# Kernel optimization log

Measured on AMD Instinct MI355X. Metric: run time of the kernel, lower is better.

## Reference

```python
import jax, jax.numpy as jnp
import numpy as np

X_DIM, Y_DIM, HIDDEN, N = 768, 768, 300, 768


def setup_inputs() -> dict:
    key = jax.random.key(0)
    ks = jax.random.split(key, 7)
    lim1 = 1.0 / np.sqrt(X_DIM + Y_DIM)
    lim2 = 1.0 / np.sqrt(HIDDEN)
    return {
        "x_samples": jax.random.normal(ks[0], (N, X_DIM), dtype=jnp.float32),
        "y_samples": jax.random.normal(ks[1], (N, Y_DIM), dtype=jnp.float32),
        "perm": jax.random.permutation(ks[2], N).astype(jnp.int32),
        # Linear 1: (x_dim+y_dim) -> hidden, torch default uniform init
        "W1": jax.random.uniform(ks[3], (HIDDEN, X_DIM + Y_DIM), jnp.float32, -lim1, lim1),
        "b1": jax.random.uniform(ks[4], (HIDDEN,), jnp.float32, -lim1, lim1),
        # Linear 2: hidden -> 1
        "W2": jax.random.uniform(ks[5], (1, HIDDEN), jnp.float32, -lim2, lim2),
        "b2": jax.random.uniform(ks[6], (1,), jnp.float32, -lim2, lim2),
    }


def reference(x_samples, y_samples, perm, W1, b1, W2, b2):
    n = x_samples.shape[0]
    x_dim = x_samples.shape[1]
    # First linear is separable across the concat: split W1 into x- and y-parts.
    hx = x_samples @ W1[:, :x_dim].T            # [N, H]
    hy = y_samples @ W1[:, x_dim:].T            # [N, H]
    w2 = W2[0]                                   # [H]
    # T0: matched pairs (x_i, y_i)
    t0 = jax.nn.softplus(jax.nn.relu(hx + hy + b1) @ w2 + b2[0])   # [N]
    # T1[i, j] = F(x_j, y_perm[i]) -- pairwise tile, [N, N, H] intermediate
    hyp = hy[perm]                               # [N, H]
    hpair = jax.nn.relu(hyp[:, None, :] + hx[None, :, :] + b1)     # [N, N, H]
    t1 = jax.nn.softplus(hpair @ w2 + b2[0])     # [N, N]
    lower_bound = t0.mean() - (jax.nn.logsumexp(t1, axis=1).mean() - jnp.log(n).astype(t1.dtype))
    return lower_bound
```

## Files before the change

### kernel.cpp

```cpp
#include <hip/hip_runtime.h>
#include <math.h>

#define NN   768
#define HH   300
#define HPAD 320
#define KD   768

#define P_OFF    0
#define PKS_STR  245760
#define PG_STR   1966080
#define CF_OFF   3932160
#define AF_OFF   4177920
#define SP_OFF   4423680
#define SP_STR   589824
#define ES_OFF   6782976
#define T0_OFF   6783744

__global__ __launch_bounds__(256) void k1_gemm(
    const float* __restrict__ x, const float* __restrict__ y,
    const int* __restrict__ perm, const float* __restrict__ W1,
    float* __restrict__ wsf)
{
    const int tid = threadIdx.x;
    const int tx = tid & 15;
    const int ty = tid >> 4;
    const int i0 = blockIdx.x * 128;
    const int h0 = blockIdx.y * 64;
    const int g  = blockIdx.z & 1;
    const int ks = blockIdx.z >> 1;
    const int kbeg = ks * 96;

    const float* src = g ? y : x;
    const int koff = g ? KD : 0;

    __shared__ float Xt[32][132];
    __shared__ float Wt[32][68];

    float4 acc[4][2];
    #pragma unroll
    for (int r = 0; r < 4; ++r) { acc[r][0] = make_float4(0,0,0,0);
                                  acc[r][1] = make_float4(0,0,0,0); }

    const int kq = (tid & 7) << 2;
    const float* xp[4];
    int xr[4];
    #pragma unroll
    for (int it = 0; it < 4; ++it) {
        int row = ((tid + it*256) >> 3);
        int gr = i0 + row;
        if (g) gr = perm[gr];
        xp[it] = src + (size_t)gr * KD + kbeg + kq;
        xr[it] = row;
    }
    const float* wp[2];
    int wr[2]; bool wv[2];
    #pragma unroll
    for (int it = 0; it < 2; ++it) {
        int hrow = ((tid + it*256) >> 3);
        int hg = h0 + hrow;
        wv[it] = hg < HH;
        wp[it] = W1 + (size_t)(wv[it] ? hg : 0) * (2*KD) + koff + kbeg + kq;
        wr[it] = hrow;
    }

    for (int kb = 0; kb < 96; kb += 32) {
        float4 xv[4], wvv[2];
        #pragma unroll
        for (int it = 0; it < 4; ++it) xv[it] = *(const float4*)(xp[it] + kb);
        #pragma unroll
        for (int it = 0; it < 2; ++it) {
            wvv[it] = *(const float4*)(wp[it] + kb);
            if (!wv[it]) wvv[it] = make_float4(0,0,0,0);
        }
        if (kb) __syncthreads();
        #pragma unroll
        for (int it = 0; it < 4; ++it) {
            Xt[kq+0][xr[it]] = xv[it].x; Xt[kq+1][xr[it]] = xv[it].y;
            Xt[kq+2][xr[it]] = xv[it].z; Xt[kq+3][xr[it]] = xv[it].w;
        }
        #pragma unroll
        for (int it = 0; it < 2; ++it) {
            Wt[kq+0][wr[it]] = wvv[it].x; Wt[kq+1][wr[it]] = wvv[it].y;
            Wt[kq+2][wr[it]] = wvv[it].z; Wt[kq+3][wr[it]] = wvv[it].w;
        }
        __syncthreads();

        #pragma unroll 8
        for (int k = 0; k < 32; ++k) {
            float4 a  = *(const float4*)&Wt[k][4*ty];
            float4 b0 = *(const float4*)&Xt[k][4*tx];
            float4 b1v = *(const float4*)&Xt[k][64 + 4*tx];
            float ar[4] = {a.x, a.y, a.z, a.w};
            #pragma unroll
            for (int r = 0; r < 4; ++r) {
                acc[r][0].x = fmaf(ar[r], b0.x,  acc[r][0].x);
                acc[r][0].y = fmaf(ar[r], b0.y,  acc[r][0].y);
                acc[r][0].z = fmaf(ar[r], b0.z,  acc[r][0].z);
                acc[r][0].w = fmaf(ar[r], b0.w,  acc[r][0].w);
                acc[r][1].x = fmaf(ar[r], b1v.x, acc[r][1].x);
                acc[r][1].y = fmaf(ar[r], b1v.y, acc[r][1].y);
                acc[r][1].z = fmaf(ar[r], b1v.z, acc[r][1].z);
                acc[r][1].w = fmaf(ar[r], b1v.w, acc[r][1].w);
            }
        }
    }

    float* dst = wsf + P_OFF + (size_t)(g*8 + ks) * PKS_STR;
    #pragma unroll
    for (int r = 0; r < 4; ++r) {
        float* rp = dst + (size_t)(h0 + 4*ty + r) * NN + i0;
        *(float4*)(rp + 4*tx)      = acc[r][0];
        *(float4*)(rp + 64 + 4*tx) = acc[r][1];
    }
}

__global__ __launch_bounds__(256) void k1b_combine(
    const float* __restrict__ b1, float* __restrict__ wsf)
{
    int idx = blockIdx.x * 256 + threadIdx.x;
    int g = idx >= 61440;
    int rem = idx - g * 61440;
    int h = rem / 192;
    int i4 = (rem % 192) * 4;

    float4 o = make_float4(0.f,0.f,0.f,0.f);
    if (h < HH) {
        const float* p = wsf + P_OFF + (size_t)g * PG_STR + (size_t)h * NN + i4;
        #pragma unroll
        for (int ks = 0; ks < 8; ++ks) {
            float4 v = *(const float4*)(p + (size_t)ks * PKS_STR);
            o.x += v.x; o.y += v.y; o.z += v.z; o.w += v.w;
        }
        if (g) {
            float bv = b1[h];
            o.x += bv; o.y += bv; o.z += bv; o.w += bv;
        }
    }
    float* dst = wsf + (g ? AF_OFF : CF_OFF) + (size_t)h * NN + i4;
    *(float4*)dst = o;
}

__global__ __launch_bounds__(256) void k2_pair(
    const float* __restrict__ wsf, const float* __restrict__ w2,
    float* __restrict__ sp)
{
    const int tid = threadIdx.x;
    const int tx = tid & 15;
    const int ty = tid >> 4;
    const int j0 = blockIdx.x * 48;
    const int i0 = blockIdx.y * 96;
    const int p  = blockIdx.z;
    const int h0 = p * 75;

    const float* AF = wsf + AF_OFF;
    const float* CF = wsf + CF_OFF;

    __shared__ float As[75][100];
    __shared__ float Cs[75][48];
    __shared__ float w2s[75];

    for (int e = tid; e < 1800; e += 256) {
        int h = e / 24, q = (e % 24) * 4;
        float4 v = *(const float4*)(AF + (size_t)(h0 + h) * NN + i0 + q);
        *(float4*)&As[h][q] = v;
    }
    for (int e = tid; e < 900; e += 256) {
        int h = e / 12, q = (e % 12) * 4;
        float4 v = *(const float4*)(CF + (size_t)(h0 + h) * NN + j0 + q);
        *(float4*)&Cs[h][q] = v;
    }
    if (tid < 75) w2s[tid] = w2[h0 + tid];
    __syncthreads();

    float acc[6][3];
    #pragma unroll
    for (int r = 0; r < 6; ++r)
        #pragma unroll
        for (int c = 0; c < 3; ++c) acc[r][c] = 0.f;

    #pragma unroll 5
    for (int h = 0; h < 75; ++h) {
        float wh = w2s[h];
        float4 a0 = *(const float4*)&As[h][4*ty];
        float2 a1 = *(const float2*)&As[h][64 + 2*ty];
        float2 c0 = *(const float2*)&Cs[h][2*tx];
        float  c2 = Cs[h][32 + tx];
        float ar[6] = {a0.x, a0.y, a0.z, a0.w, a1.x, a1.y};
        float cr[3] = {c0.x, c0.y, c2};
        #pragma unroll
        for (int r = 0; r < 6; ++r) {
            #pragma unroll
            for (int c = 0; c < 3; ++c) {
                float t = fmaxf(ar[r] + cr[c], 0.f);
                acc[r][c] = fmaf(t, wh, acc[r][c]);
            }
        }
    }

    float* dst = sp + (size_t)p * SP_STR;
    #pragma unroll
    for (int r = 0; r < 6; ++r) {
        int i = i0 + ((r < 4) ? (4*ty + r) : (64 + 2*ty + (r - 4)));
        float* rp = dst + (size_t)i * NN + j0;
        *(float2*)(rp + 2*tx) = make_float2(acc[r][0], acc[r][1]);
        rp[32 + tx] = acc[r][2];
    }
}

__global__ __launch_bounds__(256) void k2e_rows(
    const float* __restrict__ wsf, const int* __restrict__ perm,
    const float* __restrict__ w2, const float* __restrict__ b2,
    float* __restrict__ esum, float* __restrict__ t0out)
{
    const int tid = threadIdx.x;
    const float b2v = b2[0];

    if ((int)blockIdx.x < NN) {
        __shared__ float red[256];
        const int row = blockIdx.x;
        const float* spr = wsf + SP_OFF + (size_t)row * NN;
        float e = 0.f;
        #pragma unroll
        for (int jj = 0; jj < 3; ++jj) {
            int j = tid + jj * 256;
            float s = spr[j];
            s += spr[(size_t)1 * SP_STR + j];
            s += spr[(size_t)2 * SP_STR + j];
            s += spr[(size_t)3 * SP_STR + j];
            e += expf(s + b2v);
        }
        red[tid] = e;
        __syncthreads();
        for (int s = 128; s > 0; s >>= 1) {
            if (tid < s) red[tid] += red[tid + s];
            __syncthreads();
        }
        if (tid == 0) esum[row] = red[0];
    } else {
        const int col = ((int)blockIdx.x - NN) * 256 + tid;
        const int pcol = perm[col];
        const float* AF = wsf + AF_OFF;
        const float* CF = wsf + CF_OFF;
        float s = 0.f;
        for (int h = 0; h < HH; ++h) {
            float a = AF[(size_t)h * NN + col];
            float c = CF[(size_t)h * NN + pcol];
            float z = fmaxf(a + c, 0.f);
            s = fmaf(z, w2[h], s);
        }
        float u = s + b2v;
        t0out[col] = (u > 0.f) ? u + log1pf(expf(-u)) : log1pf(expf(u));
    }
}

__global__ __launch_bounds__(256) void k3_final(
    const float* __restrict__ wsf, float* __restrict__ out)
{
    const int tid = threadIdx.x;
    const float* esum = wsf + ES_OFF;
    const float* t0   = wsf + T0_OFF;

    double st0 = 0.0, slse = 0.0;
    for (int i = tid; i < NN; i += 256) {
        st0  += (double)t0[i];
        slse += log((double)NN + (double)esum[i]);
    }
    __shared__ double sa[256], sb[256];
    sa[tid] = st0; sb[tid] = slse;
    __syncthreads();
    for (int s = 128; s > 0; s >>= 1) {
        if (tid < s) { sa[tid] += sa[tid+s]; sb[tid] += sb[tid+s]; }
        __syncthreads();
    }
    if (tid == 0) {
        double lb = sa[0]/(double)NN - (sb[0]/(double)NN - log((double)NN));
        out[0] = (float)lb;
    }
}

extern "C" void kernel_launch(void* const* d_in, const int* in_sizes, int n_in,
                              void* d_out, int out_size, void* d_ws, size_t ws_size,
                              hipStream_t stream) {
    const float* x    = (const float*)d_in[0];
    const float* y    = (const float*)d_in[1];
    const int*   perm = (const int*)  d_in[2];
    const float* W1   = (const float*)d_in[3];
    const float* b1   = (const float*)d_in[4];
    const float* W2   = (const float*)d_in[5];
    const float* b2   = (const float*)d_in[6];
    float* wsf = (float*)d_ws;
    float* out = (float*)d_out;

    k1_gemm    <<<dim3(6,5,16), 256, 0, stream>>>(x, y, perm, W1, wsf);
    k1b_combine<<<480,          256, 0, stream>>>(b1, wsf);
    k2_pair    <<<dim3(16,8,4), 256, 0, stream>>>(wsf, W2, wsf + SP_OFF);
    k2e_rows   <<<NN + 3,       256, 0, stream>>>(wsf, perm, W2, b2,
                                                  wsf + ES_OFF, wsf + T0_OFF);
    k3_final   <<<1,            256, 0, stream>>>(wsf, out);
}
```

Baseline: 135.3 us.

## Retile pairwise kernel with 8-way hidden split and fuse final reduction via atomics

The pairwise kernel now uses 64x128 output tiles with 4x8 register blocks per thread and splits the hidden dimension into 8 slices of 38, giving 576 blocks instead of 512. The padded rows past 300 get zero weights. The row-sum kernel sums 8 partial slices and accumulates the logsumexp and t0 totals into double atomics, with a last-block counter writing the output. This removes the separate final kernel launch. The cost is twice the partial-sum memory traffic and some atomic contention.

```diff
diff --git a/kernel.cpp b/kernel.cpp
--- a/kernel.cpp
+++ b/kernel.cpp
@@ -13,8 +13,7 @@
 #define AF_OFF   4177920
 #define SP_OFF   4423680
 #define SP_STR   589824
-#define ES_OFF   6782976
-#define T0_OFF   6783744
+#define ACC_OFF  9142272
 
 __global__ __launch_bounds__(256) void k1_gemm(
     const float* __restrict__ x, const float* __restrict__ y,
@@ -118,6 +117,11 @@
     const float* __restrict__ b1, float* __restrict__ wsf)
 {
     int idx = blockIdx.x * 256 + threadIdx.x;
+    if (idx == 0) {
+        double* accd = (double*)(wsf + ACC_OFF);
+        accd[0] = 0.0; accd[1] = 0.0;
+        *(unsigned int*)(wsf + ACC_OFF + 4) = 0u;
+    }
     int g = idx >= 61440;
     int rem = idx - g * 61440;
     int h = rem / 192;
@@ -147,50 +151,50 @@
     const int tid = threadIdx.x;
     const int tx = tid & 15;
     const int ty = tid >> 4;
-    const int j0 = blockIdx.x * 48;
-    const int i0 = blockIdx.y * 96;
+    const int j0 = blockIdx.x * 128;
+    const int i0 = blockIdx.y * 64;
     const int p  = blockIdx.z;
-    const int h0 = p * 75;
+    const int h0 = p * 38;
 
     const float* AF = wsf + AF_OFF;
     const float* CF = wsf + CF_OFF;
 
-    __shared__ float As[75][100];
-    __shared__ float Cs[75][48];
-    __shared__ float w2s[75];
-
-    for (int e = tid; e < 1800; e += 256) {
-        int h = e / 24, q = (e % 24) * 4;
-        float4 v = *(const float4*)(AF + (size_t)(h0 + h) * NN + i0 + q);
-        *(float4*)&As[h][q] = v;
-    }
-    for (int e = tid; e < 900; e += 256) {
-        int h = e / 12, q = (e % 12) * 4;
-        float4 v = *(const float4*)(CF + (size_t)(h0 + h) * NN + j0 + q);
-        *(float4*)&Cs[h][q] = v;
-    }
-    if (tid < 75) w2s[tid] = w2[h0 + tid];
+    __shared__ float As[38][68];
+    __shared__ float Cs[38][132];
+    __shared__ float w2s[38];
+
+    for (int e = tid; e < 608; e += 256) {
+        int h = e >> 4, q = (e & 15) * 4;
+        *(float4*)&As[h][q] = *(const float4*)(AF + (size_t)(h0 + h) * NN + i0 + q);
+    }
+    for (int e = tid; e < 1216; e += 256) {
+        int h = e >> 5, q = (e & 31) * 4;
+        *(float4*)&Cs[h][q] = *(const float4*)(CF + (size_t)(h0 + h) * NN + j0 + q);
+    }
+    if (tid < 38) {
+        int h = h0 + tid;
+        w2s[tid] = (h < HH) ? w2[h] : 0.f;
+    }
     __syncthreads();
 
-    float acc[6][3];
-    #pragma unroll
-    for (int r = 0; r < 6; ++r)
-        #pragma unroll
-        for (int c = 0; c < 3; ++c) acc[r][c] = 0.f;
-
-    #pragma unroll 5
-    for (int h = 0; h < 75; ++h) {
+    float acc[4][8];
+    #pragma unroll
+    for (int r = 0; r < 4; ++r)
+        #pragma unroll
+        for (int c = 0; c < 8; ++c) acc[r][c] = 0.f;
+
+    #pragma unroll 2
+    for (int h = 0; h < 38; ++h) {
         float wh = w2s[h];
-        float4 a0 = *(const float4*)&As[h][4*ty];
-        float2 a1 = *(const float2*)&As[h][64 + 2*ty];
-        float2 c0 = *(const float2*)&Cs[h][2*tx];
-        float  c2 = Cs[h][32 + tx];
-        float ar[6] = {a0.x, a0.y, a0.z, a0.w, a1.x, a1.y};
-        float cr[3] = {c0.x, c0.y, c2};
-        #pragma unroll
-        for (int r = 0; r < 6; ++r) {
+        float4 av = *(const float4*)&As[h][4*ty];
+        float4 c0 = *(const float4*)&Cs[h][4*tx];
+        float4 c1 = *(const float4*)&Cs[h][64 + 4*tx];
+        float ar[4] = {av.x, av.y, av.z, av.w};
+        float cr[8] = {c0.x, c0.y, c0.z, c0.w, c1.x, c1.y, c1.z, c1.w};
+        #pragma unroll
+        for (int r = 0; r < 4; ++r) {
             #pragma unroll
-            for (int c = 0; c < 3; ++c) {
+            for (int c = 0; c < 8; ++c) {
                 float t = fmaxf(ar[r] + cr[c], 0.f);
                 acc[r][c] = fmaf(t, wh, acc[r][c]);
             }
@@ -199,34 +203,36 @@
 
     float* dst = sp + (size_t)p * SP_STR;
     #pragma unroll
-    for (int r = 0; r < 6; ++r) {
-        int i = i0 + ((r < 4) ? (4*ty + r) : (64 + 2*ty + (r - 4)));
-        float* rp = dst + (size_t)i * NN + j0;
-        *(float2*)(rp + 2*tx) = make_float2(acc[r][0], acc[r][1]);
-        rp[32 + tx] = acc[r][2];
+    for (int r = 0; r < 4; ++r) {
+        float* rp = dst + (size_t)(i0 + 4*ty + r) * NN + j0;
+        *(float4*)(rp + 4*tx) =
+            make_float4(acc[r][0], acc[r][1], acc[r][2], acc[r][3]);
+        *(float4*)(rp + 64 + 4*tx) =
+            make_float4(acc[r][4], acc[r][5], acc[r][6], acc[r][7]);
     }
 }
 
 __global__ __launch_bounds__(256) void k2e_rows(
     const float* __restrict__ wsf, const int* __restrict__ perm,
     const float* __restrict__ w2, const float* __restrict__ b2,
-    float* __restrict__ esum, float* __restrict__ t0out)
+    float* __restrict__ wsmut, float* __restrict__ out)
 {
     const int tid = threadIdx.x;
     const float b2v = b2[0];
+    double* accd = (double*)(wsmut + ACC_OFF);
+    unsigned int* cnt = (unsigned int*)(wsmut + ACC_OFF + 4);
+    __shared__ float red[256];
 
     if ((int)blockIdx.x < NN) {
-        __shared__ float red[256];
         const int row = blockIdx.x;
         const float* spr = wsf + SP_OFF + (size_t)row * NN;
         float e = 0.f;
         #pragma unroll
         for (int jj = 0; jj < 3; ++jj) {
             int j = tid + jj * 256;
-            float s = spr[j];
-            s += spr[(size_t)1 * SP_STR + j];
-            s += spr[(size_t)2 * SP_STR + j];
-            s += spr[(size_t)3 * SP_STR + j];
+            float s = 0.f;
+            #pragma unroll
+            for (int p = 0; p < 8; ++p) s += spr[(size_t)p * SP_STR + j];
             e += expf(s + b2v);
         }
         red[tid] = e;
@@ -235,13 +241,15 @@
             if (tid < s) red[tid] += red[tid + s];
             __syncthreads();
         }
-        if (tid == 0) esum[row] = red[0];
+        if (tid == 0)
+            atomicAdd(&accd[1], log((double)NN + (double)red[0]));
     } else {
         const int col = ((int)blockIdx.x - NN) * 256 + tid;
         const int pcol = perm[col];
         const float* AF = wsf + AF_OFF;
         const float* CF = wsf + CF_OFF;
         float s = 0.f;
+        #pragma unroll 4
         for (int h = 0; h < HH; ++h) {
             float a = AF[(size_t)h * NN + col];
             float c = CF[(size_t)h * NN + pcol];
@@ -249,32 +257,26 @@
             s = fmaf(z, w2[h], s);
         }
         float u = s + b2v;
-        t0out[col] = (u > 0.f) ? u + log1pf(expf(-u)) : log1pf(expf(u));
-    }
-}
-
-__global__ __launch_bounds__(256) void k3_final(
-    const float* __restrict__ wsf, float* __restrict__ out)
-{
-    const int tid = threadIdx.x;
-    const float* esum = wsf + ES_OFF;
-    const float* t0   = wsf + T0_OFF;
-
-    double st0 = 0.0, slse = 0.0;
-    for (int i = tid; i < NN; i += 256) {
-        st0  += (double)t0[i];
-        slse += log((double)NN + (double)esum[i]);
-    }
-    __shared__ double sa[256], sb[256];
-    sa[tid] = st0; sb[tid] = slse;
-    __syncthreads();
-    for (int s = 128; s > 0; s >>= 1) {
-        if (tid < s) { sa[tid] += sa[tid+s]; sb[tid] += sb[tid+s]; }
+        red[tid] = (u > 0.f) ? u + log1pf(expf(-u)) : log1pf(expf(u));
         __syncthreads();
-    }
+        for (int sh = 128; sh > 0; sh >>= 1) {
+            if (tid < sh) red[tid] += red[tid + sh];
+            __syncthreads();
+        }
+        if (tid == 0)
+            atomicAdd(&accd[0], (double)red[0]);
+    }
+
     if (tid == 0) {
-        double lb = sa[0]/(double)NN - (sb[0]/(double)NN - log((double)NN));
-        out[0] = (float)lb;
+        __threadfence();
+        unsigned int old = atomicAdd(cnt, 1u);
+        if (old == (unsigned int)(NN + 3 - 1)) {
+            double st0  = atomicAdd(&accd[0], 0.0);
+            double slse = atomicAdd(&accd[1], 0.0);
+            double lb = st0 / (double)NN
+                      - (slse / (double)NN - log((double)NN));
+            out[0] = (float)lb;
+        }
     }
 }
 
@@ -291,10 +293,8 @@
     float* wsf = (float*)d_ws;
     float* out = (float*)d_out;
 
-    k1_gemm    <<<dim3(6,5,16), 256, 0, stream>>>(x, y, perm, W1, wsf);
-    k1b_combine<<<480,          256, 0, stream>>>(b1, wsf);
-    k2_pair    <<<dim3(16,8,4), 256, 0, stream>>>(wsf, W2, wsf + SP_OFF);
-    k2e_rows   <<<NN + 3,       256, 0, stream>>>(wsf, perm, W2, b2,
-                                                  wsf + ES_OFF, wsf + T0_OFF);
-    k3_final   <<<1,            256, 0, stream>>>(wsf, out);
-}
+    k1_gemm    <<<dim3(6,5,16),  256, 0, stream>>>(x, y, perm, W1, wsf);
+    k1b_combine<<<480,           256, 0, stream>>>(b1, wsf);
+    k2_pair    <<<dim3(6,12,8),  256, 0, stream>>>(wsf, W2, wsf + SP_OFF);
+    k2e_rows   <<<NN + 3,        256, 0, stream>>>(wsf, perm, W2, b2, wsf, out);
+}
```

After: 163.9 us. +21.2%, slower.
